# Kernel tuning notes

Measured on AMD Instinct MI355X. Metric: run time of the kernel, lower is better.

The kernel has to match this reference:

```python
import jax, jax.numpy as jnp
import numpy as np

N_NODES = 100000
N_EDGES = 1000000
N_LABEL = 200000
D_IN = 128
D_HID = 128


def setup_inputs() -> dict:
    key = jax.random.key(0)
    k1, k2, k3, k4, k5 = jax.random.split(key, 5)
    node_feature = jax.random.normal(k1, (N_NODES, D_IN), dtype=jnp.float32)
    edge_index = jax.random.randint(k2, (2, N_EDGES), 0, N_NODES, dtype=jnp.int64)
    edge_label_index = jax.random.randint(k3, (2, N_LABEL), 0, N_NODES, dtype=jnp.int64)
    W1 = jax.random.normal(k4, (D_IN, D_HID), dtype=jnp.float32) * (1.0 / np.sqrt(D_IN))
    b1 = jnp.zeros((D_HID,), dtype=jnp.float32)
    W2 = jax.random.normal(k5, (D_HID, D_HID), dtype=jnp.float32) * (1.0 / np.sqrt(D_HID))
    b2 = jnp.zeros((D_HID,), dtype=jnp.float32)
    return {"node_feature": node_feature, "edge_index": edge_index,
            "edge_label_index": edge_label_index,
            "W1": W1, "b1": b1, "W2": W2, "b2": b2}


def reference(node_feature, edge_index, edge_label_index, W1, b1, W2, b2):
    N = node_feature.shape[0]
    # GCN normalization with added self-loops (PyG GCNConv default)
    loop = jnp.arange(N, dtype=edge_index.dtype)
    src = jnp.concatenate([edge_index[0], loop])  # [E+N]
    dst = jnp.concatenate([edge_index[1], loop])  # [E+N]
    deg = jax.ops.segment_sum(jnp.ones_like(dst, dtype=node_feature.dtype), dst, N)
    dinv = jnp.where(deg > 0, jax.lax.rsqrt(deg), 0.0)
    norm = dinv[src] * dinv[dst]  # [E+N]

    def gcn_conv(x, W, b):
        h = x @ W                              # [N, d] transform first (d small)
        msg = h[src] * norm[:, None]           # gather + scale over edges
        return jax.ops.segment_sum(msg, dst, N) + b  # scatter-add to targets

    # eval mode: dropout(p=0.2) is identity
    x = jax.nn.relu(gcn_conv(node_feature, W1, b1))
    x = gcn_conv(x, W2, b2)

    # edge scoring: gather both endpoints, elementwise mul, sum over features
    nodes_first = x[edge_label_index[0]]
    nodes_second = x[edge_label_index[1]]
    pred = jnp.sum(nodes_first * nodes_second, axis=-1)  # [N_LABEL]
    return pred
```

## Files before the change

### kernel.cpp

```cpp
#include <hip/hip_runtime.h>
#include <hip/hip_bf16.h>


#define N_NODES 100000
#define N_EDGES 1000000
#define N_LABEL 200000
#define D_FEAT 128
#define BM 128

#define NB 782
#define BCAP 2048
#define P1_EPT 16
#define P1_BLOCKS 245
#define G_GEMM 782
#define G_CONV 128

typedef short bf16x8 __attribute__((ext_vector_type(8)));
typedef float f32x4 __attribute__((ext_vector_type(4)));

__device__ inline unsigned int f2bf(float x) {
    unsigned int u = __float_as_uint(x);
    return (u + 0x7FFFu + ((u >> 16) & 1u)) >> 16;
}
__device__ inline unsigned int bf16pack(float a, float b) {
    return f2bf(a) | (f2bf(b) << 16);
}
__device__ inline float bflo(unsigned int u) { return __uint_as_float(u << 16); }
__device__ inline float bfhi(unsigned int u) { return __uint_as_float(u & 0xFFFF0000u); }

__global__ __launch_bounds__(256) void w2bf(
    const float* __restrict__ W1, const float* __restrict__ W2,
    unsigned short* __restrict__ Wt1, unsigned short* __restrict__ Wt2) {
    int i = blockIdx.x * 256 + threadIdx.x;
    const float* W = (i < 16384) ? W1 : W2;
    unsigned short* Wt = (i < 16384) ? Wt1 : Wt2;
    int j = i & 16383;
    int n = j >> 7, k = j & 127;
    Wt[j] = (unsigned short)f2bf(W[(size_t)k * 128 + n]);
}

template <bool BF16_IN>
__device__ __forceinline__ void gemm_body(const void* __restrict__ Xv,
                                          const unsigned short* __restrict__ Wt,
                                          unsigned int* __restrict__ Y,
                                          int nrows, int bid, short* Ws) {
    int t = threadIdx.x;
#pragma unroll
    for (int i = 0; i < 8; ++i) {
        int c = i * 256 + t;
        int n = c >> 4, q = c & 15;
        uint4 v = *(const uint4*)&Wt[(size_t)n * 128 + q * 8];
        *(uint4*)&Ws[n * 128 + ((q ^ (n & 15)) << 3)] = v;
    }
    __syncthreads();

    int wv = t >> 6;
    int lane = t & 63, l16 = lane & 15, quad = lane >> 4;
    int rbase = bid * BM + wv * 32;

    f32x4 acc[2][8];
#pragma unroll
    for (int rt = 0; rt < 2; ++rt)
#pragma unroll
        for (int nt = 0; nt < 8; ++nt) acc[rt][nt] = (f32x4){0.f, 0.f, 0.f, 0.f};

#pragma unroll
    for (int kb = 0; kb < 4; ++kb) {
        bf16x8 af[2];
#pragma unroll
        for (int rt = 0; rt < 2; ++rt) {
            int row = rbase + rt * 16 + l16;
            if (row > nrows - 1) row = nrows - 1;
            if constexpr (BF16_IN) {
                const unsigned int* Xb = (const unsigned int*)Xv;
                af[rt] = *(const bf16x8*)&Xb[(size_t)row * 64 + kb * 16 + quad * 4];
            } else {
                const float* X = (const float*)Xv;
                float4 fa = ((const float4*)X)[(size_t)row * 32 + kb * 8 + quad * 2];
                float4 fb = ((const float4*)X)[(size_t)row * 32 + kb * 8 + quad * 2 + 1];
                union { uint4 u; bf16x8 v; } cv;
                cv.u.x = bf16pack(fa.x, fa.y);
                cv.u.y = bf16pack(fa.z, fa.w);
                cv.u.z = bf16pack(fb.x, fb.y);
                cv.u.w = bf16pack(fb.z, fb.w);
                af[rt] = cv.v;
            }
        }
        bf16x8 bfr[8];
#pragma unroll
        for (int nt = 0; nt < 8; ++nt) {
            int n = nt * 16 + l16;
            bfr[nt] = *(const bf16x8*)&Ws[n * 128 + (((kb * 4 + quad) ^ l16) << 3)];
        }
#pragma unroll
        for (int rt = 0; rt < 2; ++rt)
#pragma unroll
            for (int nt = 0; nt < 8; ++nt)
                acc[rt][nt] = __builtin_amdgcn_mfma_f32_16x16x32_bf16(
                    af[rt], bfr[nt], acc[rt][nt], 0, 0, 0);
    }

    short* Ys = (short*)Y;
#pragma unroll
    for (int rt = 0; rt < 2; ++rt)
#pragma unroll
        for (int reg = 0; reg < 4; ++reg) {
            int row = rbase + rt * 16 + quad * 4 + reg;
            if (row < nrows) {
#pragma unroll
                for (int nt = 0; nt < 8; ++nt)
                    Ys[(size_t)row * 128 + nt * 16 + l16] = (short)f2bf(acc[rt][nt][reg]);
            }
        }
}

__global__ __launch_bounds__(256) void gemm128_mfma_bf16(const unsigned int* __restrict__ Xb,
                                                         const unsigned short* __restrict__ Wt,
                                                         unsigned int* __restrict__ Y,
                                                         int nrows) {
    __shared__ __align__(16) short Ws[128 * 128];
    gemm_body<true>(Xb, Wt, Y, nrows, blockIdx.x, Ws);
}

__global__ __launch_bounds__(256) void fused_gemm1_pass1(
    const float* __restrict__ feat, const unsigned short* __restrict__ wt1,
    unsigned int* __restrict__ Hb,
    const int* __restrict__ src, const int* __restrict__ dst,
    unsigned int* __restrict__ temp, int* __restrict__ bofs) {
    __shared__ __align__(16) short Ws[128 * 128];
    int b = blockIdx.x, t = threadIdx.x;
    if (b < G_GEMM) {
        gemm_body<false>(feat, wt1, Hb, N_NODES, b, Ws);
        return;
    }
    b -= G_GEMM;
    unsigned int* ed16 = (unsigned int*)Ws;
    int* hist = (int*)(ed16 + 4096);
    int* red = hist + 1024;

    for (int i = t; i < 1024; i += 256) hist[i] = 0;
    __syncthreads();

    int se[P1_EPT], de[P1_EPT], rk[P1_EPT];
    int e0 = b * 4096 + t;
#pragma unroll
    for (int j = 0; j < P1_EPT; ++j) {
        int e = e0 + j * 256;
        if (e < N_EDGES) {
            se[j] = src[e];
            de[j] = dst[e];
            rk[j] = atomicAdd(&hist[de[j] >> 7], 1);
        }
    }
    __syncthreads();

    int c0 = hist[4 * t], c1 = hist[4 * t + 1], c2 = hist[4 * t + 2], c3 = hist[4 * t + 3];
    int s = c0 + c1 + c2 + c3;
    red[t] = s;
    __syncthreads();
    for (int off = 1; off < 256; off <<= 1) {
        int a = (t >= off) ? red[t - off] : 0;
        __syncthreads();
        red[t] += a;
        __syncthreads();
    }
    int excl = red[t] - s;
    hist[4 * t] = excl;
    hist[4 * t + 1] = excl + c0;
    hist[4 * t + 2] = excl + c0 + c1;
    hist[4 * t + 3] = excl + c0 + c1 + c2;
    __syncthreads();

#pragma unroll
    for (int j = 0; j < P1_EPT; ++j) {
        int e = e0 + j * 256;
        if (e < N_EDGES) {
            int pos = hist[de[j] >> 7] + rk[j];
            ed16[pos] = (unsigned int)(((de[j] & 127) << 17) | se[j]);
        }
    }
    __syncthreads();

#pragma unroll
    for (int i = 0; i < 4; ++i)
        ((uint4*)temp)[(size_t)b * 1024 + i * 256 + t] = ((uint4*)ed16)[i * 256 + t];
    for (int j = t; j < NB; j += 256) bofs[b * (NB + 1) + j] = hist[j];
    if (t == 0) {
        int cnt = N_EDGES - b * 4096;
        if (cnt > 4096) cnt = 4096;
        bofs[b * (NB + 1) + NB] = cnt;
    }
}

__global__ __launch_bounds__(256) void pass2_sort(
    const unsigned int* __restrict__ temp, const int* __restrict__ bofs,
    int* __restrict__ row_ptr, float* __restrict__ dinv,
    int* __restrict__ packed) {
    int k = blockIdx.x, t = threadIdx.x;
    __shared__ unsigned int ed[BCAP];
    __shared__ int hist[128], rp[128], cur[128], sc2[128];
    __shared__ int red[256], sc[256];

    int s_t = 0, len = 0;
    if (t < P1_BLOCKS) {
        s_t = bofs[t * (NB + 1) + k];
        len = bofs[t * (NB + 1) + k + 1] - s_t;
    }
    red[t] = s_t;
    __syncthreads();
    for (int off = 128; off > 0; off >>= 1) {
        if (t < off) red[t] += red[t + off];
        __syncthreads();
    }
    int gbase = red[0];
    __syncthreads();
    sc[t] = len;
    __syncthreads();
    for (int off = 1; off < 256; off <<= 1) {
        int a = (t >= off) ? sc[t - off] : 0;
        __syncthreads();
        sc[t] += a;
        __syncthreads();
    }
    int dloc = sc[t] - len;
    int nk = sc[255];
    if (nk > BCAP) nk = BCAP;

    if (t < 128) { hist[t] = 0; cur[t] = 0; }
    __syncthreads();
    for (int i = 0; i < len; ++i) {
        int d = dloc + i;
        if (d < BCAP) ed[d] = temp[(size_t)t * 4096 + s_t + i];
    }
    __syncthreads();
    for (int i = t; i < nk; i += 256) atomicAdd(&hist[ed[i] >> 17], 1);
    __syncthreads();

    if (t < 128) sc2[t] = hist[t];
    __syncthreads();
    for (int off = 1; off < 128; off <<= 1) {
        int a = (t < 128 && t >= off) ? sc2[t - off] : 0;
        __syncthreads();
        if (t < 128) sc2[t] += a;
        __syncthreads();
    }
    if (t < 128) {
        rp[t] = sc2[t] - hist[t];
        int n = k * 128 + t;
        if (n < N_NODES) {
            row_ptr[n] = gbase + rp[t];
            dinv[n] = rsqrtf((float)(hist[t] + 1));
        }
    }
    if (k == NB - 1 && t == 0) row_ptr[N_NODES] = N_EDGES;
    __syncthreads();

    for (int i = t; i < nk; i += 256) {
        unsigned int v = ed[i];
        int dl = v >> 17;
        int r = atomicAdd(&cur[dl], 1);
        packed[gbase + rp[dl] + r] = (int)(v & 0x1FFFF);
    }
}

template <bool RELU>
__global__ __launch_bounds__(256) void aggregate(const unsigned int* __restrict__ Hb,
                                                 const int* __restrict__ packed,
                                                 const int* __restrict__ row_ptr,
                                                 const float* __restrict__ dinv,
                                                 const float* __restrict__ bias,
                                                 unsigned int* __restrict__ Xb) {
    int v0 = blockIdx.x * 8 + (threadIdx.x >> 6) * 2;
    int v1 = v0 + 1;
    int lane = threadIdx.x & 63;
    if (v0 >= N_NODES) return;
    bool h1 = (v1 < N_NODES);

    int st0 = row_ptr[v0], en0 = row_ptr[v0 + 1];
    int st1 = h1 ? row_ptr[v1] : 0, en1 = h1 ? row_ptr[v1 + 1] : 0;
    float dv0 = dinv[v0];
    float dv1 = h1 ? dinv[v1] : 0.f;

    unsigned int su0 = Hb[(size_t)v0 * 64 + lane];
    float a0 = dv0 * bflo(su0), a1 = dv0 * bfhi(su0);
    unsigned int su1 = h1 ? Hb[(size_t)v1 * 64 + lane] : 0u;
    float b0 = dv1 * bflo(su1), b1 = dv1 * bfhi(su1);

    int p = 0;
    if (lane < 32) {
        if (st0 + lane < en0) p = packed[st0 + lane];
    } else {
        if (st1 + lane - 32 < en1) p = packed[st1 + lane - 32];
    }

    for (int c0 = st0, c1 = st1; c0 < en0 || c1 < en1; c0 += 32, c1 += 32) {
        int n0 = en0 - c0; n0 = n0 < 0 ? 0 : (n0 > 32 ? 32 : n0);
        int n1 = en1 - c1; n1 = n1 < 0 ? 0 : (n1 > 32 ? 32 : n1);
        bool act = (lane < 32) ? (lane < n0) : (lane - 32 < n1);
        float dld = dinv[p];
        float d = act ? dld : 0.f;

        int nmax = n0 > n1 ? n0 : n1;
        int pn = 0;
        bool pref = false;
        for (int j = 0; j < nmax; j += 8) {
            int sA[8], sB[8];
#pragma unroll
            for (int q = 0; q < 8; ++q) {
                sA[q] = __shfl(p, j + q);
                sB[q] = __shfl(p, 32 + j + q);
            }
            unsigned int uA[8], uB[8];
#pragma unroll
            for (int q = 0; q < 8; ++q) {
                uA[q] = Hb[(size_t)sA[q] * 64 + lane];
                uB[q] = Hb[(size_t)sB[q] * 64 + lane];
            }
            if (!pref) {
                pref = true;
                if (lane < 32) {
                    if (c0 + 32 + lane < en0) pn = packed[c0 + 32 + lane];
                } else {
                    if (c1 + lane < en1) pn = packed[c1 + lane];
                }
            }
            float dA[8], dB[8];
#pragma unroll
            for (int q = 0; q < 8; ++q) {
                dA[q] = __shfl(d, j + q);
                dB[q] = __shfl(d, 32 + j + q);
            }
#pragma unroll
            for (int q = 0; q < 8; ++q) {
                a0 = fmaf(dA[q], bflo(uA[q]), a0);
                a1 = fmaf(dA[q], bfhi(uA[q]), a1);
                b0 = fmaf(dB[q], bflo(uB[q]), b0);
                b1 = fmaf(dB[q], bfhi(uB[q]), b1);
            }
        }
        p = pn;
    }

    float2 bb = ((const float2*)bias)[lane];
    a0 = fmaf(a0, dv0, bb.x);
    a1 = fmaf(a1, dv0, bb.y);
    b0 = fmaf(b0, dv1, bb.x);
    b1 = fmaf(b1, dv1, bb.y);
    if (RELU) {
        a0 = fmaxf(a0, 0.f);
        a1 = fmaxf(a1, 0.f);
        b0 = fmaxf(b0, 0.f);
        b1 = fmaxf(b1, 0.f);
    }
    Xb[(size_t)v0 * 64 + lane] = bf16pack(a0, a1);
    if (h1) Xb[(size_t)v1 * 64 + lane] = bf16pack(b0, b1);
}

__global__ __launch_bounds__(256) void score_kernel(const int* __restrict__ ea,
                                                    const int* __restrict__ eb,
                                                    const unsigned int* __restrict__ Xb,
                                                    float* __restrict__ out) {
    int wbase = (blockIdx.x * 4 + (threadIdx.x >> 6)) * 4;
    int lane = threadIdx.x & 63;
    if (wbase >= N_LABEL) return;
    int ne = N_LABEL - wbase;
    if (ne > 4) ne = 4;

    unsigned int ua[4], ub[4];
#pragma unroll
    for (int e = 0; e < 4; ++e)
        if (e < ne) {
            int ia = ea[wbase + e], ib = eb[wbase + e];
            ua[e] = Xb[(size_t)ia * 64 + lane];
            ub[e] = Xb[(size_t)ib * 64 + lane];
        }
#pragma unroll
    for (int e = 0; e < 4; ++e)
        if (e < ne) {
            float p = bflo(ua[e]) * bflo(ub[e]) + bfhi(ua[e]) * bfhi(ub[e]);
#pragma unroll
            for (int off = 32; off > 0; off >>= 1) p += __shfl_down(p, off);
            if (lane == 0) out[wbase + e] = p;
        }
}

extern "C" void kernel_launch(void* const* d_in, const int* in_sizes, int n_in,
                              void* d_out, int out_size, void* d_ws, size_t ws_size,
                              hipStream_t stream) {
    const float* feat = (const float*)d_in[0];
    const int* ei = (const int*)d_in[1];
    const int* eli = (const int*)d_in[2];
    const float* W1 = (const float*)d_in[3];
    const float* b1 = (const float*)d_in[4];
    const float* W2 = (const float*)d_in[5];
    const float* b2 = (const float*)d_in[6];
    float* out = (float*)d_out;

    const int* src = ei;
    const int* dst = ei + N_EDGES;
    const int* la = eli;
    const int* lb = eli + N_LABEL;

    int* row_ptr = (int*)d_ws;
    float* dinv = (float*)(row_ptr + N_NODES + 4);
    unsigned short* wt1 = (unsigned short*)(dinv + N_NODES);
    unsigned short* wt2 = wt1 + 16384;
    int* packed = (int*)(wt2 + 16384);
    unsigned int* Hb = (unsigned int*)(packed + N_EDGES);
    unsigned int* Xb = Hb + (size_t)N_NODES * 64;
    unsigned int* temp = Xb;
    int* bofs = (int*)(temp + (size_t)P1_BLOCKS * 4096);

    const int TB = 256;
    int gGemm = (N_NODES + BM - 1) / BM;
    int gAgg = (N_NODES + 7) / 8;
    int gScore = (N_LABEL + 15) / 16;

    w2bf<<<G_CONV, TB, 0, stream>>>(W1, W2, wt1, wt2);

    fused_gemm1_pass1<<<G_GEMM + P1_BLOCKS, TB, 0, stream>>>(
        feat, wt1, Hb, src, dst, temp, bofs);

    pass2_sort<<<NB, TB, 0, stream>>>(temp, bofs, row_ptr, dinv, packed);

    aggregate<true><<<gAgg, TB, 0, stream>>>(Hb, packed, row_ptr, dinv, b1, Xb);

    gemm128_mfma_bf16<<<gGemm, TB, 0, stream>>>(Xb, wt2, Hb, N_NODES);
    aggregate<false><<<gAgg, TB, 0, stream>>>(Hb, packed, row_ptr, dinv, b2, Xb);

    score_kernel<<<gScore, TB, 0, stream>>>(la, lb, Xb, out);
}
```

Baseline: 278.4 us.

## Regroup launches: fuse weight conversion with pass1, GEMM1 with pass2 sort

Moves the edge-bucketing pass1 into the weight-conversion kernel and merges the GEMM1 with the pass2 bucket sort as independent block ranges of one launch. This cuts one kernel launch and lets the short pass2 sort overlap with the GEMM instead of running serially after it. The pass2 shared arrays are now carved out of the GEMM's 32KB Ws buffer. The cost is that pass1 now runs alongside only a small conversion job rather than beside GEMM1.

New measurement: 275.5 us, median of 2. About the same (-1.1%).

```diff
diff --git a/kernel.cpp b/kernel.cpp
--- a/kernel.cpp
+++ b/kernel.cpp
@@ -28,15 +28,79 @@
 __device__ inline float bflo(unsigned int u) { return __uint_as_float(u << 16); }
 __device__ inline float bfhi(unsigned int u) { return __uint_as_float(u & 0xFFFF0000u); }
 
-__global__ __launch_bounds__(256) void w2bf(
+__global__ __launch_bounds__(256) void w2bf_pass1(
     const float* __restrict__ W1, const float* __restrict__ W2,
-    unsigned short* __restrict__ Wt1, unsigned short* __restrict__ Wt2) {
-    int i = blockIdx.x * 256 + threadIdx.x;
-    const float* W = (i < 16384) ? W1 : W2;
-    unsigned short* Wt = (i < 16384) ? Wt1 : Wt2;
-    int j = i & 16383;
-    int n = j >> 7, k = j & 127;
-    Wt[j] = (unsigned short)f2bf(W[(size_t)k * 128 + n]);
+    unsigned short* __restrict__ Wt1, unsigned short* __restrict__ Wt2,
+    const int* __restrict__ src, const int* __restrict__ dst,
+    unsigned int* __restrict__ temp, int* __restrict__ bofs) {
+    __shared__ __align__(16) unsigned int S[4096 + 1024 + 256];
+    int b = blockIdx.x, t = threadIdx.x;
+    if (b < G_CONV) {
+        int i = b * 256 + t;
+        const float* W = (i < 16384) ? W1 : W2;
+        unsigned short* Wt = (i < 16384) ? Wt1 : Wt2;
+        int j = i & 16383;
+        int n = j >> 7, k = j & 127;
+        Wt[j] = (unsigned short)f2bf(W[(size_t)k * 128 + n]);
+        return;
+    }
+    b -= G_CONV;
+    unsigned int* ed16 = S;
+    int* hist = (int*)(ed16 + 4096);
+    int* red = hist + 1024;
+
+    for (int i = t; i < 1024; i += 256) hist[i] = 0;
+    __syncthreads();
+
+    int se[P1_EPT], de[P1_EPT], rk[P1_EPT];
+    int e0 = b * 4096 + t;
+#pragma unroll
+    for (int j = 0; j < P1_EPT; ++j) {
+        int e = e0 + j * 256;
+        if (e < N_EDGES) {
+            se[j] = src[e];
+            de[j] = dst[e];
+            rk[j] = atomicAdd(&hist[de[j] >> 7], 1);
+        }
+    }
+    __syncthreads();
+
+    int c0 = hist[4 * t], c1 = hist[4 * t + 1], c2 = hist[4 * t + 2], c3 = hist[4 * t + 3];
+    int s = c0 + c1 + c2 + c3;
+    red[t] = s;
+    __syncthreads();
+    for (int off = 1; off < 256; off <<= 1) {
+        int a = (t >= off) ? red[t - off] : 0;
+        __syncthreads();
+        red[t] += a;
+        __syncthreads();
+    }
+    int excl = red[t] - s;
+    hist[4 * t] = excl;
+    hist[4 * t + 1] = excl + c0;
+    hist[4 * t + 2] = excl + c0 + c1;
+    hist[4 * t + 3] = excl + c0 + c1 + c2;
+    __syncthreads();
+
+#pragma unroll
+    for (int j = 0; j < P1_EPT; ++j) {
+        int e = e0 + j * 256;
+        if (e < N_EDGES) {
+            int pos = hist[de[j] >> 7] + rk[j];
+            ed16[pos] = (unsigned int)(((de[j] & 127) << 17) | se[j]);
+        }
+    }
+    __syncthreads();
+
+#pragma unroll
+    for (int i = 0; i < 4; ++i)
+        ((uint4*)temp)[(size_t)b * 1024 + i * 256 + t] = ((uint4*)ed16)[i * 256 + t];
+    for (int j = t; j < NB; j += 256) bofs[b * (NB + 1) + j] = hist[j];
+    if (t == 0) {
+        int cnt = N_EDGES - b * 4096;
+        if (cnt > 4096) cnt = 4096;
+        bofs[b * (NB + 1) + NB] = cnt;
+    }
 }
 
 template <bool BF16_IN>
@@ -122,84 +186,26 @@
     gemm_body<true>(Xb, Wt, Y, nrows, blockIdx.x, Ws);
 }
 
-__global__ __launch_bounds__(256) void fused_gemm1_pass1(
+__global__ __launch_bounds__(256) void fused_gemm1_pass2(
     const float* __restrict__ feat, const unsigned short* __restrict__ wt1,
     unsigned int* __restrict__ Hb,
-    const int* __restrict__ src, const int* __restrict__ dst,
-    unsigned int* __restrict__ temp, int* __restrict__ bofs) {
+    const unsigned int* __restrict__ temp, const int* __restrict__ bofs,
+    int* __restrict__ row_ptr, float* __restrict__ dinv,
+    int* __restrict__ packed) {
     __shared__ __align__(16) short Ws[128 * 128];
     int b = blockIdx.x, t = threadIdx.x;
     if (b < G_GEMM) {
         gemm_body<false>(feat, wt1, Hb, N_NODES, b, Ws);
         return;
     }
-    b -= G_GEMM;
-    unsigned int* ed16 = (unsigned int*)Ws;
-    int* hist = (int*)(ed16 + 4096);
-    int* red = hist + 1024;
-
-    for (int i = t; i < 1024; i += 256) hist[i] = 0;
-    __syncthreads();
-
-    int se[P1_EPT], de[P1_EPT], rk[P1_EPT];
-    int e0 = b * 4096 + t;
-#pragma unroll
-    for (int j = 0; j < P1_EPT; ++j) {
-        int e = e0 + j * 256;
-        if (e < N_EDGES) {
-            se[j] = src[e];
-            de[j] = dst[e];
-            rk[j] = atomicAdd(&hist[de[j] >> 7], 1);
-        }
-    }
-    __syncthreads();
-
-    int c0 = hist[4 * t], c1 = hist[4 * t + 1], c2 = hist[4 * t + 2], c3 = hist[4 * t + 3];
-    int s = c0 + c1 + c2 + c3;
-    red[t] = s;
-    __syncthreads();
-    for (int off = 1; off < 256; off <<= 1) {
-        int a = (t >= off) ? red[t - off] : 0;
-        __syncthreads();
-        red[t] += a;
-        __syncthreads();
-    }
-    int excl = red[t] - s;
-    hist[4 * t] = excl;
-    hist[4 * t + 1] = excl + c0;
-    hist[4 * t + 2] = excl + c0 + c1;
-    hist[4 * t + 3] = excl + c0 + c1 + c2;
-    __syncthreads();
-
-#pragma unroll
-    for (int j = 0; j < P1_EPT; ++j) {
-        int e = e0 + j * 256;
-        if (e < N_EDGES) {
-            int pos = hist[de[j] >> 7] + rk[j];
-            ed16[pos] = (unsigned int)(((de[j] & 127) << 17) | se[j]);
-        }
-    }
-    __syncthreads();
-
-#pragma unroll
-    for (int i = 0; i < 4; ++i)
-        ((uint4*)temp)[(size_t)b * 1024 + i * 256 + t] = ((uint4*)ed16)[i * 256 + t];
-    for (int j = t; j < NB; j += 256) bofs[b * (NB + 1) + j] = hist[j];
-    if (t == 0) {
-        int cnt = N_EDGES - b * 4096;
-        if (cnt > 4096) cnt = 4096;
-        bofs[b * (NB + 1) + NB] = cnt;
-    }
-}
-
-__global__ __launch_bounds__(256) void pass2_sort(
-    const unsigned int* __restrict__ temp, const int* __restrict__ bofs,
-    int* __restrict__ row_ptr, float* __restrict__ dinv,
-    int* __restrict__ packed) {
-    int k = blockIdx.x, t = threadIdx.x;
-    __shared__ unsigned int ed[BCAP];
-    __shared__ int hist[128], rp[128], cur[128], sc2[128];
-    __shared__ int red[256], sc[256];
+    int k = b - G_GEMM;
+    unsigned int* ed = (unsigned int*)Ws;
+    int* hist = (int*)(ed + BCAP);
+    int* rp = hist + 128;
+    int* cur = rp + 128;
+    int* sc2 = cur + 128;
+    int* red = sc2 + 128;
+    int* sc = red + 256;
 
     int s_t = 0, len = 0;
     if (t < P1_BLOCKS) {
@@ -416,12 +422,11 @@
     int gAgg = (N_NODES + 7) / 8;
     int gScore = (N_LABEL + 15) / 16;
 
-    w2bf<<<G_CONV, TB, 0, stream>>>(W1, W2, wt1, wt2);
-
-    fused_gemm1_pass1<<<G_GEMM + P1_BLOCKS, TB, 0, stream>>>(
-        feat, wt1, Hb, src, dst, temp, bofs);
-
-    pass2_sort<<<NB, TB, 0, stream>>>(temp, bofs, row_ptr, dinv, packed);
+    w2bf_pass1<<<G_CONV + P1_BLOCKS, TB, 0, stream>>>(W1, W2, wt1, wt2,
+                                                      src, dst, temp, bofs);
+
+    fused_gemm1_pass2<<<G_GEMM + NB, TB, 0, stream>>>(
+        feat, wt1, Hb, temp, bofs, row_ptr, dinv, packed);
 
     aggregate<true><<<gAgg, TB, 0, stream>>>(Hb, packed, row_ptr, dinv, b1, Xb);
 
```
